# Optimization experiments

Hardware: AMD Instinct MI355X
Metric: run time of the kernel (lower is better)

Reference implementation:

```python
import jax, jax.numpy as jnp
import numpy as np

N_QUBITS = 4
N_LAYERS = 6
BATCH = 262144


def _apply_1q(state, U, wire):
    """Apply a 1-qubit gate U ((2,2) shared or (B,2,2) per-sample) on `wire`.
    state: (B, 2, 2, ..., 2) with n qubit axes after the batch axis."""
    s = jnp.moveaxis(state, 1 + wire, -1)
    shp = s.shape
    s2 = s.reshape(shp[0], -1, 2)
    if U.ndim == 3:
        s2 = jnp.einsum('bij,bkj->bki', U, s2)
    else:
        s2 = jnp.einsum('ij,bkj->bki', U, s2)
    return jnp.moveaxis(s2.reshape(shp), -1, 1 + wire)


def _apply_cnot(state, control, target):
    s = jnp.moveaxis(state, (1 + control, 1 + target), (-2, -1))
    shp = s.shape
    s2 = s.reshape(shp[0], -1, 2, 2)
    # flip target amplitudes where control bit is 1
    s2 = jnp.stack([s2[..., 0, :], s2[..., 1, ::-1]], axis=-2)
    return jnp.moveaxis(s2.reshape(shp), (-2, -1), (1 + control, 1 + target))


def _ry_batched(x):
    """RY(x) for x: (B,) -> (B,2,2) complex64 (real-valued matrix)."""
    c, s = jnp.cos(x / 2), jnp.sin(x / 2)
    m = jnp.stack([jnp.stack([c, -s], -1), jnp.stack([s, c], -1)], -2)
    return m.astype(jnp.complex64)


def _rot(phi, theta, omega):
    """qml.Rot = RZ(omega) RY(theta) RZ(phi), (2,2) complex64."""
    c, s = jnp.cos(theta / 2), jnp.sin(theta / 2)
    e = lambda a: jnp.exp(1j * a)
    m00 = e(-(phi + omega) / 2) * c
    m01 = -e((phi - omega) / 2) * s
    m10 = e(-(phi - omega) / 2) * s
    m11 = e((phi + omega) / 2) * c
    return jnp.stack([jnp.stack([m00, m01]), jnp.stack([m10, m11])]).astype(jnp.complex64)


def setup_inputs() -> dict:
    key = jax.random.key(0)
    k1, k2 = jax.random.split(key)
    inputs = jax.random.normal(k1, (BATCH, N_QUBITS), dtype=jnp.float32)
    quantum_weights = jax.random.uniform(k2, (N_LAYERS, N_QUBITS, 3), dtype=jnp.float32, minval=-0.05, maxval=0.05)
    return {"inputs": inputs, "quantum_weights": quantum_weights}


def reference(inputs, quantum_weights):
    B, n = inputs.shape
    L = quantum_weights.shape[0]
    # |0...0> state, batched
    state = jnp.zeros((B,) + (2,) * n, jnp.complex64)
    state = state.at[(slice(None),) + (0,) * n].set(1.0)
    # AngleEmbedding(rotation='Y'): RY(inputs[:, w]) on wire w
    for w in range(n):
        state = _apply_1q(state, _ry_batched(inputs[:, w]), w)
    # StronglyEntanglingLayers: Rot per wire, then ring of CNOTs with range r = l % (n-1) + 1
    for l in range(L):
        for w in range(n):
            state = _apply_1q(state, _rot(quantum_weights[l, w, 0], quantum_weights[l, w, 1], quantum_weights[l, w, 2]), w)
        r = l % (n - 1) + 1
        for w in range(n):
            state = _apply_cnot(state, w, (w + r) % n)
    # <Z_w> for each wire
    p = jnp.abs(state.reshape(B, -1)) ** 2  # (B, 2^n)
    bits = (jnp.arange(2 ** n)[:, None] >> jnp.arange(n - 1, -1, -1)[None, :]) & 1
    z = (1 - 2 * bits).astype(p.dtype)  # (2^n, n)
    return p @ z  # (B, n) float32
```

## Files before the change

### kernel.cpp

```cpp
#include <hip/hip_runtime.h>

#define N_QUBITS 4
#define N_LAYERS 6
#define NSTATES  16

__device__ __forceinline__ float2 cmul(float2 a, float2 b) {
    return make_float2(a.x * b.x - a.y * b.y, a.x * b.y + a.y * b.x);
}
__device__ __forceinline__ float2 cadd(float2 a, float2 b) {
    return make_float2(a.x + b.x, a.y + b.y);
}

__global__ __launch_bounds__(256) void qc_kernel(
        const float* __restrict__ inputs,
        const float* __restrict__ weights,
        float* __restrict__ out,
        int B) {
    __shared__ float2 rotm[N_LAYERS][N_QUBITS][4];

    const int t = threadIdx.x;
    if (t < N_LAYERS * N_QUBITS) {
        const int l = t / N_QUBITS, w = t % N_QUBITS;
        const float phi   = weights[(l * N_QUBITS + w) * 3 + 0];
        const float theta = weights[(l * N_QUBITS + w) * 3 + 1];
        const float omega = weights[(l * N_QUBITS + w) * 3 + 2];
        float st, ct;
        sincosf(theta * 0.5f, &st, &ct);
        const float a1 = -(phi + omega) * 0.5f;
        const float a2 =  (phi - omega) * 0.5f;
        float s1, c1, s2, c2;
        sincosf(a1, &s1, &c1);
        sincosf(a2, &s2, &c2);
        rotm[l][w][0] = make_float2( c1 * ct,  s1 * ct);
        rotm[l][w][1] = make_float2(-c2 * st, -s2 * st);
        rotm[l][w][2] = make_float2( c2 * st, -s2 * st);
        rotm[l][w][3] = make_float2( c1 * ct, -s1 * ct);
    }
    __syncthreads();

    const int b = blockIdx.x * blockDim.x + t;
    if (b >= B) return;

    const float4 xin = reinterpret_cast<const float4*>(inputs)[b];
    float cc[N_QUBITS], ss[N_QUBITS];
    sincosf(xin.x * 0.5f, &ss[0], &cc[0]);
    sincosf(xin.y * 0.5f, &ss[1], &cc[1]);
    sincosf(xin.z * 0.5f, &ss[2], &cc[2]);
    sincosf(xin.w * 0.5f, &ss[3], &cc[3]);

    float2 amp[NSTATES];
    #pragma unroll
    for (int i = 0; i < NSTATES; ++i) {
        float v = 1.0f;
        #pragma unroll
        for (int w = 0; w < N_QUBITS; ++w)
            v *= ((i >> (3 - w)) & 1) ? ss[w] : cc[w];
        amp[i] = make_float2(v, 0.0f);
    }

    #pragma unroll
    for (int l = 0; l < N_LAYERS; ++l) {
        #pragma unroll
        for (int w = 0; w < N_QUBITS; ++w) {
            const int bit = 1 << (3 - w);
            const float2 m00 = rotm[l][w][0];
            const float2 m01 = rotm[l][w][1];
            const float2 m10 = rotm[l][w][2];
            const float2 m11 = rotm[l][w][3];
            #pragma unroll
            for (int i = 0; i < NSTATES; ++i) {
                if (!(i & bit)) {
                    const int j = i | bit;
                    const float2 a0 = amp[i];
                    const float2 a1v = amp[j];
                    amp[i] = cadd(cmul(m00, a0), cmul(m01, a1v));
                    amp[j] = cadd(cmul(m10, a0), cmul(m11, a1v));
                }
            }
        }
        const int r = l % (N_QUBITS - 1) + 1;
        #pragma unroll
        for (int w = 0; w < N_QUBITS; ++w) {
            const int cbit = 1 << (3 - w);
            const int tbit = 1 << (3 - ((w + r) % N_QUBITS));
            #pragma unroll
            for (int i = 0; i < NSTATES; ++i) {
                if ((i & cbit) && !(i & tbit)) {
                    const int j = i | tbit;
                    const float2 tmp = amp[i];
                    amp[i] = amp[j];
                    amp[j] = tmp;
                }
            }
        }
    }

    float z0 = 0.f, z1 = 0.f, z2 = 0.f, z3 = 0.f;
    #pragma unroll
    for (int i = 0; i < NSTATES; ++i) {
        const float p = amp[i].x * amp[i].x + amp[i].y * amp[i].y;
        z0 += ((i >> 3) & 1) ? -p : p;
        z1 += ((i >> 2) & 1) ? -p : p;
        z2 += ((i >> 1) & 1) ? -p : p;
        z3 += ((i >> 0) & 1) ? -p : p;
    }
    reinterpret_cast<float4*>(out)[b] = make_float4(z0, z1, z2, z3);
}

extern "C" void kernel_launch(void* const* d_in, const int* in_sizes, int n_in,
                              void* d_out, int out_size, void* d_ws, size_t ws_size,
                              hipStream_t stream) {
    const float* inputs  = (const float*)d_in[0];
    const float* weights = (const float*)d_in[1];
    float* out = (float*)d_out;
    const int B = in_sizes[0] / N_QUBITS;
    const int block = 256;
    const int grid = (B + block - 1) / block;
    qc_kernel<<<grid, block, 0, stream>>>(inputs, weights, out, B);
}
```

Baseline: 83.93 us.

## Precompute fused 16x16 circuit unitary once, apply as real-input matvec per sample

Every sample shares the same weight-dependent gates, so a tiny single-block kernel now builds the full 16x16 complex unitary of all entangling layers into workspace. The main kernel builds the real product-state amplitudes from the RY angles and applies that unitary as a real-by-complex matvec, which cuts per-sample gate work. It also switches to fast __sincosf and uses a butterfly reduction for the Z expectations. The cost is an extra kernel launch and 512 uniform float loads from global memory per thread, plus some accuracy loss from the fast sincos.

```diff
diff --git a/kernel.cpp b/kernel.cpp
--- a/kernel.cpp
+++ b/kernel.cpp
@@ -11,11 +11,8 @@
     return make_float2(a.x + b.x, a.y + b.y);
 }
 
-__global__ __launch_bounds__(256) void qc_kernel(
-        const float* __restrict__ inputs,
-        const float* __restrict__ weights,
-        float* __restrict__ out,
-        int B) {
+__global__ void build_u_kernel(const float* __restrict__ weights,
+                               float* __restrict__ U) {
     __shared__ float2 rotm[N_LAYERS][N_QUBITS][4];
 
     const int t = threadIdx.x;
@@ -38,72 +35,115 @@
     }
     __syncthreads();
 
-    const int b = blockIdx.x * blockDim.x + t;
+    if (t < NSTATES) {
+        float2 amp[NSTATES];
+        #pragma unroll
+        for (int i = 0; i < NSTATES; ++i)
+            amp[i] = make_float2(i == t ? 1.0f : 0.0f, 0.0f);
+
+        #pragma unroll
+        for (int l = 0; l < N_LAYERS; ++l) {
+            #pragma unroll
+            for (int w = 0; w < N_QUBITS; ++w) {
+                const int bit = 1 << (3 - w);
+                const float2 m00 = rotm[l][w][0];
+                const float2 m01 = rotm[l][w][1];
+                const float2 m10 = rotm[l][w][2];
+                const float2 m11 = rotm[l][w][3];
+                #pragma unroll
+                for (int i = 0; i < NSTATES; ++i) {
+                    if (!(i & bit)) {
+                        const int j = i | bit;
+                        const float2 a0 = amp[i];
+                        const float2 a1v = amp[j];
+                        amp[i] = cadd(cmul(m00, a0), cmul(m01, a1v));
+                        amp[j] = cadd(cmul(m10, a0), cmul(m11, a1v));
+                    }
+                }
+            }
+            const int r = l % (N_QUBITS - 1) + 1;
+            #pragma unroll
+            for (int w = 0; w < N_QUBITS; ++w) {
+                const int cbit = 1 << (3 - w);
+                const int tbit = 1 << (3 - ((w + r) % N_QUBITS));
+                #pragma unroll
+                for (int i = 0; i < NSTATES; ++i) {
+                    if ((i & cbit) && !(i & tbit)) {
+                        const int j = i | tbit;
+                        const float2 tmp = amp[i];
+                        amp[i] = amp[j];
+                        amp[j] = tmp;
+                    }
+                }
+            }
+        }
+
+        #pragma unroll
+        for (int i = 0; i < NSTATES; ++i) {
+            U[2 * (i * NSTATES + t) + 0] = amp[i].x;
+            U[2 * (i * NSTATES + t) + 1] = amp[i].y;
+        }
+    }
+}
+
+__global__ __launch_bounds__(256) void qc_apply_kernel(
+        const float* __restrict__ inputs,
+        const float* __restrict__ U,
+        float* __restrict__ out,
+        int B) {
+    const int b = blockIdx.x * blockDim.x + threadIdx.x;
     if (b >= B) return;
 
     const float4 xin = reinterpret_cast<const float4*>(inputs)[b];
-    float cc[N_QUBITS], ss[N_QUBITS];
-    sincosf(xin.x * 0.5f, &ss[0], &cc[0]);
-    sincosf(xin.y * 0.5f, &ss[1], &cc[1]);
-    sincosf(xin.z * 0.5f, &ss[2], &cc[2]);
-    sincosf(xin.w * 0.5f, &ss[3], &cc[3]);
+    float s0, c0, s1, c1, s2, c2, s3, c3;
+    __sincosf(xin.x * 0.5f, &s0, &c0);
+    __sincosf(xin.y * 0.5f, &s1, &c1);
+    __sincosf(xin.z * 0.5f, &s2, &c2);
+    __sincosf(xin.w * 0.5f, &s3, &c3);
 
-    float2 amp[NSTATES];
+    float vA[4] = { c0 * c1, c0 * s1, s0 * c1, s0 * s1 };
+    float vB[4] = { c2 * c3, c2 * s3, s2 * c3, s2 * s3 };
+    float v[NSTATES];
+    #pragma unroll
+    for (int a = 0; a < 4; ++a)
+        #pragma unroll
+        for (int q = 0; q < 4; ++q)
+            v[a * 4 + q] = vA[a] * vB[q];
+
+    float p[NSTATES];
     #pragma unroll
     for (int i = 0; i < NSTATES; ++i) {
-        float v = 1.0f;
+        float re = 0.0f, im = 0.0f;
         #pragma unroll
-        for (int w = 0; w < N_QUBITS; ++w)
-            v *= ((i >> (3 - w)) & 1) ? ss[w] : cc[w];
-        amp[i] = make_float2(v, 0.0f);
+        for (int k = 0; k < NSTATES; ++k) {
+            const float ur = U[2 * (i * NSTATES + k) + 0];
+            const float ui = U[2 * (i * NSTATES + k) + 1];
+            re = fmaf(ur, v[k], re);
+            im = fmaf(ui, v[k], im);
+        }
+        p[i] = re * re + im * im;
     }
 
+    float s0a[8], d0a[8];
     #pragma unroll
-    for (int l = 0; l < N_LAYERS; ++l) {
-        #pragma unroll
-        for (int w = 0; w < N_QUBITS; ++w) {
-            const int bit = 1 << (3 - w);
-            const float2 m00 = rotm[l][w][0];
-            const float2 m01 = rotm[l][w][1];
-            const float2 m10 = rotm[l][w][2];
-            const float2 m11 = rotm[l][w][3];
-            #pragma unroll
-            for (int i = 0; i < NSTATES; ++i) {
-                if (!(i & bit)) {
-                    const int j = i | bit;
-                    const float2 a0 = amp[i];
-                    const float2 a1v = amp[j];
-                    amp[i] = cadd(cmul(m00, a0), cmul(m01, a1v));
-                    amp[j] = cadd(cmul(m10, a0), cmul(m11, a1v));
-                }
-            }
-        }
-        const int r = l % (N_QUBITS - 1) + 1;
-        #pragma unroll
-        for (int w = 0; w < N_QUBITS; ++w) {
-            const int cbit = 1 << (3 - w);
-            const int tbit = 1 << (3 - ((w + r) % N_QUBITS));
-            #pragma unroll
-            for (int i = 0; i < NSTATES; ++i) {
-                if ((i & cbit) && !(i & tbit)) {
-                    const int j = i | tbit;
-                    const float2 tmp = amp[i];
-                    amp[i] = amp[j];
-                    amp[j] = tmp;
-                }
-            }
-        }
+    for (int j = 0; j < 8; ++j) {
+        s0a[j] = p[2 * j] + p[2 * j + 1];
+        d0a[j] = p[2 * j] - p[2 * j + 1];
     }
+    float z3 = ((d0a[0] + d0a[1]) + (d0a[2] + d0a[3])) +
+               ((d0a[4] + d0a[5]) + (d0a[6] + d0a[7]));
+    float s1a[4], d1a[4];
+    #pragma unroll
+    for (int j = 0; j < 4; ++j) {
+        s1a[j] = s0a[2 * j] + s0a[2 * j + 1];
+        d1a[j] = s0a[2 * j] - s0a[2 * j + 1];
+    }
+    float z2 = (d1a[0] + d1a[1]) + (d1a[2] + d1a[3]);
+    float s2a0 = s1a[0] + s1a[1], s2a1 = s1a[2] + s1a[3];
+    float d2a0 = s1a[0] - s1a[1], d2a1 = s1a[2] - s1a[3];
+    float z1 = d2a0 + d2a1;
+    float z0 = s2a0 - s2a1;
 
-    float z0 = 0.f, z1 = 0.f, z2 = 0.f, z3 = 0.f;
-    #pragma unroll
-    for (int i = 0; i < NSTATES; ++i) {
-        const float p = amp[i].x * amp[i].x + amp[i].y * amp[i].y;
-        z0 += ((i >> 3) & 1) ? -p : p;
-        z1 += ((i >> 2) & 1) ? -p : p;
-        z2 += ((i >> 1) & 1) ? -p : p;
-        z3 += ((i >> 0) & 1) ? -p : p;
-    }
     reinterpret_cast<float4*>(out)[b] = make_float4(z0, z1, z2, z3);
 }
 
@@ -113,8 +153,12 @@
     const float* inputs  = (const float*)d_in[0];
     const float* weights = (const float*)d_in[1];
     float* out = (float*)d_out;
+    float* U   = (float*)d_ws;
     const int B = in_sizes[0] / N_QUBITS;
+
+    build_u_kernel<<<1, 64, 0, stream>>>(weights, U);
+
     const int block = 256;
     const int grid = (B + block - 1) / block;
-    qc_kernel<<<grid, block, 0, stream>>>(inputs, weights, out, B);
+    qc_apply_kernel<<<grid, block, 0, stream>>>(inputs, U, out, B);
 }
```

New measurement: 73.00 us. 1.15x faster.
